# Performance work log

Measured on AMD Instinct MI355X. Metric: run time of the kernel, lower is better.

## Reference

```python
import jax, jax.numpy as jnp
import numpy as np

N = 50000      # nodes
E = 800000     # edges (avg degree 16)
D_IN = 96
D_OUT = 96


def setup_inputs() -> dict:
    key = jax.random.key(0)
    k1, k2, k3, k4 = jax.random.split(key, 4)
    x = jax.random.normal(k1, (N, D_IN), dtype=jnp.float32)
    edge_index = jax.random.randint(k2, (2, E), 0, N, dtype=jnp.int32)
    scale = 1.0 / np.sqrt(D_IN)
    Wl = jax.random.normal(k3, (D_OUT, D_IN), dtype=jnp.float32) * scale  # lin_l weight (neighbors)
    bl = jnp.zeros((D_OUT,), dtype=jnp.float32)                           # lin_l bias
    Wr = jax.random.normal(k4, (D_OUT, D_IN), dtype=jnp.float32) * scale  # lin_r weight (root), no bias
    return {"x": x, "edge_index": edge_index, "Wl": Wl, "bl": bl, "Wr": Wr}


def reference(x, edge_index, Wl, bl, Wr):
    # SAGEConv (mean aggr): z = lin_l(mean_{j in N(i)} x_j) + lin_r(x_i), then ReLU.
    # Dropout p=0.0 -> identity.
    src, dst = edge_index[0], edge_index[1]  # messages flow src -> dst (PyG convention)
    msg = x[src]  # [E, D_IN] gather
    agg = jax.ops.segment_sum(msg, dst, num_segments=N)                     # [N, D_IN]
    deg = jax.ops.segment_sum(jnp.ones((E, 1), x.dtype), dst, num_segments=N)  # [N, 1]
    agg = agg / jnp.maximum(deg, 1.0)  # mean; isolated nodes -> 0
    z = agg @ Wl.T + bl + x @ Wr.T     # [N, D_OUT]
    return jax.nn.relu(z)
```

## Files before the change

### kernel.cpp

```cpp
#include <hip/hip_runtime.h>
#include <hip/hip_bf16.h>

#define D 96
#define CAP 32
#define NB1 256
#define BUKSHIFT 5
#define BUKN 32
#define CAPB 1024
#define NBUK_MAX 2048
#define OVL_MAX 256

typedef __attribute__((ext_vector_type(8))) short bf16x8;
typedef __attribute__((ext_vector_type(4))) float f32x4;
typedef unsigned u32x3 __attribute__((ext_vector_type(3), aligned(4)));

__device__ __forceinline__ short f2bf(float f)
{
    union { __hip_bfloat16 h; short s; } u;
    u.h = __float2bfloat16(f);
    return u.s;
}

__device__ __forceinline__ bf16x8 load_frag(const float* p)
{
    float4 lo = *(const float4*)p;
    float4 hi = *(const float4*)(p + 4);
    bf16x8 r;
    r[0] = f2bf(lo.x); r[1] = f2bf(lo.y); r[2] = f2bf(lo.z); r[3] = f2bf(lo.w);
    r[4] = f2bf(hi.x); r[5] = f2bf(hi.y); r[6] = f2bf(hi.z); r[7] = f2bf(hi.w);
    return r;
}

__device__ __forceinline__ float bf_lo(unsigned p) { return __uint_as_float(p << 16); }
__device__ __forceinline__ float bf_hi(unsigned p) { return __uint_as_float(p & 0xFFFF0000u); }

__global__ __launch_bounds__(256) void init_hist(
    const int* __restrict__ dst, const float* __restrict__ Wl,
    const float* __restrict__ Wr, __hip_bfloat16* __restrict__ wbf,
    int* __restrict__ hist, int nbuk, int E)
{
    if (blockIdx.x >= NB1) {
        int idx = (blockIdx.x - NB1) * 256 + threadIdx.x;
        if (idx < 2304) {
            int mat = idx / 1152;
            int rem = idx - mat * 1152;
            int n  = rem / 12;
            int k8 = rem - n * 12;
            const float* Wp = mat ? Wr : Wl;
            bf16x8 v = load_frag(Wp + (size_t)n * D + k8 * 8);
            int ct = n >> 4, m = n & 15, kt = k8 >> 2, quad = k8 & 3;
            ((bf16x8*)wbf)[(mat * 18 + ct * 3 + kt) * 64 + quad * 16 + m] = v;
        }
        return;
    }
    __shared__ int h[NBUK_MAX];
    for (int i = threadIdx.x; i < nbuk; i += 256) h[i] = 0;
    __syncthreads();
    const int CS = (E + NB1 - 1) / NB1;
    const int base = blockIdx.x * CS;
    int lim = E - base; if (lim > CS) lim = CS; if (lim < 0) lim = 0;
    for (int i = threadIdx.x; i < lim; i += 256)
        atomicAdd(&h[dst[base + i] >> BUKSHIFT], 1);
    __syncthreads();
    for (int i = threadIdx.x; i < nbuk; i += 256)
        hist[blockIdx.x * nbuk + i] = h[i];
}

__global__ __launch_bounds__(256) void kpre(
    const int* __restrict__ hist, int* __restrict__ ofs,
    int* __restrict__ tot, int nbuk)
{
    __shared__ int sc[256];
    const int bu = blockIdx.x, t = threadIdx.x;
    int v = hist[t * nbuk + bu];
    sc[t] = v;
    __syncthreads();
    #pragma unroll
    for (int off = 1; off < 256; off <<= 1) {
        int x = (t >= off) ? sc[t - off] : 0;
        __syncthreads();
        sc[t] += x;
        __syncthreads();
    }
    ofs[t * nbuk + bu] = bu * CAPB + (sc[t] - v);
    if (t == 255) tot[bu] = sc[t];
}

__global__ __launch_bounds__(256) void p2_gemm(
    const int* __restrict__ src, const int* __restrict__ dst,
    const int* __restrict__ ofs, unsigned* __restrict__ ebuf,
    const float* __restrict__ x, const __hip_bfloat16* __restrict__ wbf,
    __hip_bfloat16* __restrict__ hl, float* __restrict__ hr,
    int nbuk, int N, int E)
{
    if (blockIdx.x < NB1) {
        __shared__ int mo[NBUK_MAX];
        for (int i = threadIdx.x; i < nbuk; i += 256)
            mo[i] = ofs[blockIdx.x * nbuk + i];
        __syncthreads();
        const int CS = (E + NB1 - 1) / NB1;
        const int base = blockIdx.x * CS;
        int lim = E - base; if (lim > CS) lim = CS; if (lim < 0) lim = 0;
        for (int i = threadIdx.x; i < lim; i += 256) {
            int e = base + i;
            int d = dst[e], s = src[e];
            int bu = d >> BUKSHIFT;
            int g = atomicAdd(&mo[bu], 1);
            if (g < (bu + 1) * CAPB)
                ebuf[g] = (unsigned)s | ((unsigned)(d & (BUKN - 1)) << 16);
        }
        return;
    }

    const int gk = blockIdx.x - NB1;
    const int gwave = (gk * 256 + threadIdx.x) >> 6;
    const int nrt = N / 16;
    if (gwave >= nrt) return;
    const int lane = threadIdx.x & 63;
    const int m = lane & 15, quad = lane >> 4;
    const int row = gwave * 16 + m;
    const bf16x8* wb = (const bf16x8*)wbf;

    bf16x8 a[3];
    #pragma unroll
    for (int kt = 0; kt < 3; ++kt)
        a[kt] = load_frag(x + (size_t)row * D + kt * 32 + quad * 8);

    const int orow = gwave * 16 + quad * 4;
    #pragma unroll
    for (int ct = 0; ct < 6; ++ct) {
        f32x4 accl = {0.f, 0.f, 0.f, 0.f};
        f32x4 accr = {0.f, 0.f, 0.f, 0.f};
        #pragma unroll
        for (int kt = 0; kt < 3; ++kt)
            accl = __builtin_amdgcn_mfma_f32_16x16x32_bf16(
                a[kt], wb[(ct * 3 + kt) * 64 + lane], accl, 0, 0, 0);
        #pragma unroll
        for (int kt = 0; kt < 3; ++kt)
            accr = __builtin_amdgcn_mfma_f32_16x16x32_bf16(
                a[kt], wb[(18 + ct * 3 + kt) * 64 + lane], accr, 0, 0, 0);
        int col = ct * 16 + m;
        int sl = col / 24, c = col - sl * 24;
        #pragma unroll
        for (int r = 0; r < 4; ++r) {
            int node = orow + r;
            hl[((size_t)sl * N + node) * 32 + c] = __float2bfloat16(accl[r]);
            hr[(size_t)node * D + col] = accr[r];
        }
    }
}

__global__ __launch_bounds__(256) void p3agg(
    const unsigned* __restrict__ ebuf, const int* __restrict__ tot,
    const __hip_bfloat16* __restrict__ hl, const float* __restrict__ bl,
    float* __restrict__ out, int nbuk, int N)
{
    const int xcd = blockIdx.x & 7;
    const int s  = xcd >> 1;
    const int bu = ((blockIdx.x >> 3) << 1) | (xcd & 1);
    if (bu >= nbuk) return;

    __shared__ int cl[BUKN];
    __shared__ unsigned short sl[BUKN * CAP];
    __shared__ unsigned ovl[OVL_MAX];
    __shared__ int ovc;
    const int t = threadIdx.x;
    if (t < BUKN) cl[t] = 0;
    if (t == 0) ovc = 0;
    __syncthreads();

    const int n = tot[bu];
    const unsigned* eb = ebuf + (size_t)bu * CAPB;
    for (int i = t; i < n; i += 256) {
        unsigned e = eb[i];
        int dl = e >> 16, sv = (int)(e & 0xFFFFu);
        int pos = atomicAdd(&cl[dl], 1);
        if (pos < CAP) {
            sl[dl * CAP + pos] = (unsigned short)sv;
        } else {
            int o = atomicAdd(&ovc, 1);
            if (o < OVL_MAX) ovl[o] = e;
        }
    }
    __syncthreads();

    const int wv = t >> 6, lane = t & 63;
    const int nn = lane >> 4;
    const int e4 = (lane >> 2) & 3;
    const int r  = lane & 3;
    const unsigned short* hs = (const unsigned short*)hl + (size_t)s * N * 32;
    const int o = s * 24 + r * 6;
    const float b0 = bl[o],     b1 = bl[o + 1], b2 = bl[o + 2];
    const float b3 = bl[o + 3], b4 = bl[o + 4], b5 = bl[o + 5];
    const int novc = min(ovc, OVL_MAX);

    for (int q = wv * 2; q < wv * 2 + 2; ++q) {
        const int nq = q * 4;
        const int deg = cl[nq + nn];
        const int dcm = min(deg, CAP);
        int um = max(max(cl[nq], cl[nq + 1]), max(cl[nq + 2], cl[nq + 3]));
        um = min(um, CAP);

        float a0 = 0.f, a1 = 0.f, a2 = 0.f, a3 = 0.f, a4 = 0.f, a5 = 0.f;
        #pragma unroll 2
        for (int j = 0; j < um; j += 4) {
            int idx = j + e4;
            bool act = idx < dcm;
            int nb = act ? (int)sl[(nq + nn) * CAP + idx] : 0;
            u32x3 p = *(const u32x3*)((const char*)hs + (size_t)nb * 64 + r * 12);
            float mk = act ? 1.f : 0.f;
            a0 += mk * bf_lo(p.x); a1 += mk * bf_hi(p.x);
            a2 += mk * bf_lo(p.y); a3 += mk * bf_hi(p.y);
            a4 += mk * bf_lo(p.z); a5 += mk * bf_hi(p.z);
        }
        #pragma unroll
        for (int off = 4; off <= 8; off <<= 1) {
            a0 += __shfl_xor(a0, off); a1 += __shfl_xor(a1, off);
            a2 += __shfl_xor(a2, off); a3 += __shfl_xor(a3, off);
            a4 += __shfl_xor(a4, off); a5 += __shfl_xor(a5, off);
        }
        if (e4 == 0) {
            const int node = (bu << BUKSHIFT) + nq + nn;
            if (node < N) {
                for (int k = 0; k < novc; ++k) {
                    unsigned e = ovl[k];
                    if ((int)(e >> 16) == nq + nn) {
                        int nb = (int)(e & 0xFFFFu);
                        u32x3 p = *(const u32x3*)((const char*)hs + (size_t)nb * 64 + r * 12);
                        a0 += bf_lo(p.x); a1 += bf_hi(p.x);
                        a2 += bf_lo(p.y); a3 += bf_hi(p.y);
                        a4 += bf_lo(p.z); a5 += bf_hi(p.z);
                    }
                }
                const float inv = 1.0f / fmaxf((float)deg, 1.0f);
                float* op = out + (size_t)node * D + o;
                float2 u0 = *(const float2*)op;
                float2 u1 = *(const float2*)(op + 2);
                float2 u2 = *(const float2*)(op + 4);
                u0.x = fmaxf(a0 * inv + b0 + u0.x, 0.f);
                u0.y = fmaxf(a1 * inv + b1 + u0.y, 0.f);
                u1.x = fmaxf(a2 * inv + b2 + u1.x, 0.f);
                u1.y = fmaxf(a3 * inv + b3 + u1.y, 0.f);
                u2.x = fmaxf(a4 * inv + b4 + u2.x, 0.f);
                u2.y = fmaxf(a5 * inv + b5 + u2.y, 0.f);
                *(float2*)op       = u0;
                *(float2*)(op + 2) = u1;
                *(float2*)(op + 4) = u2;
            }
        }
    }
}

extern "C" void kernel_launch(void* const* d_in, const int* in_sizes, int n_in,
                              void* d_out, int out_size, void* d_ws, size_t ws_size,
                              hipStream_t stream)
{
    const float* x  = (const float*)d_in[0];
    const int*   ei = (const int*)d_in[1];
    const float* Wl = (const float*)d_in[2];
    const float* bl = (const float*)d_in[3];
    const float* Wr = (const float*)d_in[4];
    float* out = (float*)d_out;

    const int N = in_sizes[0] / D;
    const int E = in_sizes[1] / 2;
    const int* src = ei;
    const int* dst = ei + E;
    const int nbuk = (N + BUKN - 1) >> BUKSHIFT;

    char* p = (char*)d_ws;
    __hip_bfloat16* wbf = (__hip_bfloat16*)p;    p += 36864;
    __hip_bfloat16* hl  = (__hip_bfloat16*)p;    p += (size_t)4 * N * 32 * 2;
    int* hist = (int*)p;                         p += ((size_t)NB1 * nbuk * 4 + 255) / 256 * 256;
    int* ofs = (int*)p;                          p += ((size_t)NB1 * nbuk * 4 + 255) / 256 * 256;
    int* tot = (int*)p;                          p += ((size_t)nbuk * 4 + 255) / 256 * 256;
    unsigned* ebuf = (unsigned*)p;

    init_hist<<<NB1 + 9, 256, 0, stream>>>(dst, Wl, Wr, wbf, hist, nbuk, E);

    kpre<<<nbuk, 256, 0, stream>>>(hist, ofs, tot, nbuk);

    const int nrt = N / 16;
    const int gemmb = (nrt + 3) / 4;
    p2_gemm<<<NB1 + gemmb, 256, 0, stream>>>(
        src, dst, ofs, ebuf, x, wbf, hl, out, nbuk, N, E);

    const int aggb = ((nbuk + 1) / 2) * 8;
    p3agg<<<aggb, 256, 0, stream>>>(ebuf, tot, hl, bl, out, nbuk, N);
}
```

Baseline: 141.1 us.

## Replace histogram+prefix-scan passes with per-block global atomic bucket reservation

Result: faster. 133.7 us (-5.3%).

```diff
diff --git a/kernel.cpp b/kernel.cpp
--- a/kernel.cpp
+++ b/kernel.cpp
@@ -8,6 +8,7 @@
 #define BUKN 32
 #define CAPB 1024
 #define NBUK_MAX 2048
+#define KMAX 7
 #define OVL_MAX 256
 
 typedef __attribute__((ext_vector_type(8))) short bf16x8;
@@ -34,74 +35,60 @@
 __device__ __forceinline__ float bf_lo(unsigned p) { return __uint_as_float(p << 16); }
 __device__ __forceinline__ float bf_hi(unsigned p) { return __uint_as_float(p & 0xFFFF0000u); }
 
-__global__ __launch_bounds__(256) void init_hist(
-    const int* __restrict__ dst, const float* __restrict__ Wl,
-    const float* __restrict__ Wr, __hip_bfloat16* __restrict__ wbf,
-    int* __restrict__ hist, int nbuk, int E)
-{
-    if (blockIdx.x >= NB1) {
-        int idx = (blockIdx.x - NB1) * 256 + threadIdx.x;
-        if (idx < 2304) {
-            int mat = idx / 1152;
-            int rem = idx - mat * 1152;
-            int n  = rem / 12;
-            int k8 = rem - n * 12;
-            const float* Wp = mat ? Wr : Wl;
-            bf16x8 v = load_frag(Wp + (size_t)n * D + k8 * 8);
-            int ct = n >> 4, m = n & 15, kt = k8 >> 2, quad = k8 & 3;
-            ((bf16x8*)wbf)[(mat * 18 + ct * 3 + kt) * 64 + quad * 16 + m] = v;
-        }
-        return;
-    }
-    __shared__ int h[NBUK_MAX];
-    for (int i = threadIdx.x; i < nbuk; i += 256) h[i] = 0;
-    __syncthreads();
-    const int CS = (E + NB1 - 1) / NB1;
-    const int base = blockIdx.x * CS;
-    int lim = E - base; if (lim > CS) lim = CS; if (lim < 0) lim = 0;
-    for (int i = threadIdx.x; i < lim; i += 256)
-        atomicAdd(&h[dst[base + i] >> BUKSHIFT], 1);
-    __syncthreads();
-    for (int i = threadIdx.x; i < nbuk; i += 256)
-        hist[blockIdx.x * nbuk + i] = h[i];
-}
-
-__global__ __launch_bounds__(256) void kpre(
-    const int* __restrict__ hist, int* __restrict__ ofs,
-    int* __restrict__ tot, int nbuk)
-{
-    __shared__ int sc[256];
-    const int bu = blockIdx.x, t = threadIdx.x;
-    int v = hist[t * nbuk + bu];
-    sc[t] = v;
-    __syncthreads();
-    #pragma unroll
-    for (int off = 1; off < 256; off <<= 1) {
-        int x = (t >= off) ? sc[t - off] : 0;
-        __syncthreads();
-        sc[t] += x;
-        __syncthreads();
-    }
-    ofs[t * nbuk + bu] = bu * CAPB + (sc[t] - v);
-    if (t == 255) tot[bu] = sc[t];
+__global__ __launch_bounds__(256) void init_kernel(
+    const float* __restrict__ Wl, const float* __restrict__ Wr,
+    __hip_bfloat16* __restrict__ wbf, int* __restrict__ bcnt, int nbuk)
+{
+    const int idx = blockIdx.x * 256 + threadIdx.x;
+    if (idx < nbuk) bcnt[idx] = 0;
+    if (idx < 2304) {
+        int mat = idx / 1152;
+        int rem = idx - mat * 1152;
+        int n  = rem / 12;
+        int k8 = rem - n * 12;
+        const float* Wp = mat ? Wr : Wl;
+        bf16x8 v = load_frag(Wp + (size_t)n * D + k8 * 8);
+        int ct = n >> 4, m = n & 15, kt = k8 >> 2, quad = k8 & 3;
+        ((bf16x8*)wbf)[(mat * 18 + ct * 3 + kt) * 64 + quad * 16 + m] = v;
+    }
 }
 
 __global__ __launch_bounds__(256) void p2_gemm(
     const int* __restrict__ src, const int* __restrict__ dst,
-    const int* __restrict__ ofs, unsigned* __restrict__ ebuf,
+    int* __restrict__ bcnt, unsigned* __restrict__ ebuf,
     const float* __restrict__ x, const __hip_bfloat16* __restrict__ wbf,
     __hip_bfloat16* __restrict__ hl, float* __restrict__ hr,
     int nbuk, int N, int E)
 {
     if (blockIdx.x < NB1) {
         __shared__ int mo[NBUK_MAX];
-        for (int i = threadIdx.x; i < nbuk; i += 256)
-            mo[i] = ofs[blockIdx.x * nbuk + i];
+        const int t = threadIdx.x;
+        for (int i = t; i < nbuk; i += 256) mo[i] = 0;
         __syncthreads();
         const int CS = (E + NB1 - 1) / NB1;
         const int base = blockIdx.x * CS;
         int lim = E - base; if (lim > CS) lim = CS; if (lim < 0) lim = 0;
-        for (int i = threadIdx.x; i < lim; i += 256) {
+        for (int i = t; i < lim; i += 256)
+            atomicAdd(&mo[dst[base + i] >> BUKSHIFT], 1);
+        __syncthreads();
+        int c7[KMAX], b7[KMAX];
+        #pragma unroll
+        for (int k = 0; k < KMAX; ++k) {
+            int i = t + k * 256;
+            c7[k] = (i < nbuk) ? mo[i] : 0;
+        }
+        #pragma unroll
+        for (int k = 0; k < KMAX; ++k) {
+            int i = t + k * 256;
+            b7[k] = (i < nbuk) ? atomicAdd(&bcnt[i], c7[k]) : 0;
+        }
+        #pragma unroll
+        for (int k = 0; k < KMAX; ++k) {
+            int i = t + k * 256;
+            if (i < nbuk) mo[i] = i * CAPB + b7[k];
+        }
+        __syncthreads();
+        for (int i = t; i < lim; i += 256) {
             int e = base + i;
             int d = dst[e], s = src[e];
             int bu = d >> BUKSHIFT;
@@ -151,7 +138,7 @@
 }
 
 __global__ __launch_bounds__(256) void p3agg(
-    const unsigned* __restrict__ ebuf, const int* __restrict__ tot,
+    const unsigned* __restrict__ ebuf, const int* __restrict__ bcnt,
     const __hip_bfloat16* __restrict__ hl, const float* __restrict__ bl,
     float* __restrict__ out, int nbuk, int N)
 {
@@ -169,7 +156,7 @@
     if (t == 0) ovc = 0;
     __syncthreads();
 
-    const int n = tot[bu];
+    const int n = min(bcnt[bu], CAPB);
     const unsigned* eb = ebuf + (size_t)bu * CAPB;
     for (int i = t; i < n; i += 256) {
         unsigned e = eb[i];
@@ -271,20 +258,16 @@
     char* p = (char*)d_ws;
     __hip_bfloat16* wbf = (__hip_bfloat16*)p;    p += 36864;
     __hip_bfloat16* hl  = (__hip_bfloat16*)p;    p += (size_t)4 * N * 32 * 2;
-    int* hist = (int*)p;                         p += ((size_t)NB1 * nbuk * 4 + 255) / 256 * 256;
-    int* ofs = (int*)p;                          p += ((size_t)NB1 * nbuk * 4 + 255) / 256 * 256;
-    int* tot = (int*)p;                          p += ((size_t)nbuk * 4 + 255) / 256 * 256;
+    int* bcnt = (int*)p;                         p += ((size_t)nbuk * 4 + 255) / 256 * 256;
     unsigned* ebuf = (unsigned*)p;
 
-    init_hist<<<NB1 + 9, 256, 0, stream>>>(dst, Wl, Wr, wbf, hist, nbuk, E);
-
-    kpre<<<nbuk, 256, 0, stream>>>(hist, ofs, tot, nbuk);
+    init_kernel<<<9, 256, 0, stream>>>(Wl, Wr, wbf, bcnt, nbuk);
 
     const int nrt = N / 16;
     const int gemmb = (nrt + 3) / 4;
     p2_gemm<<<NB1 + gemmb, 256, 0, stream>>>(
-        src, dst, ofs, ebuf, x, wbf, hl, out, nbuk, N, E);
+        src, dst, bcnt, ebuf, x, wbf, hl, out, nbuk, N, E);
 
     const int aggb = ((nbuk + 1) / 2) * 8;
-    p3agg<<<aggb, 256, 0, stream>>>(ebuf, tot, hl, bl, out, nbuk, N);
-}
+    p3agg<<<aggb, 256, 0, stream>>>(ebuf, bcnt, hl, bl, out, nbuk, N);
+}
```
